# Optimization experiments

Measured on AMD Instinct MI355X. Metric: run time of the kernel, lower is better.

Reference implementation:

```python
import jax, jax.numpy as jnp
import numpy as np

N = 100000
E = 1000000
F_IN = 64
HID = 64
N_CLS = 2


def setup_inputs() -> dict:
    key = jax.random.key(0)
    ks = jax.random.split(key, 8)
    x = jax.random.normal(ks[0], (N, F_IN), dtype=jnp.float32)
    edge_index = jax.random.randint(ks[1], (2, E), 0, N, dtype=jnp.int64)
    s1 = 1.0 / np.sqrt(F_IN)
    s2 = 1.0 / np.sqrt(HID)
    # PyG SAGEConv: out = lin_l(mean_aggr) + lin_r(x); lin_l has bias, lin_r does not.
    W1l = jax.random.uniform(ks[2], (HID, F_IN), jnp.float32, -s1, s1)
    b1 = jax.random.uniform(ks[3], (HID,), jnp.float32, -s1, s1)
    W1r = jax.random.uniform(ks[4], (HID, F_IN), jnp.float32, -s1, s1)
    W2l = jax.random.uniform(ks[5], (N_CLS, HID), jnp.float32, -s2, s2)
    b2 = jax.random.uniform(ks[6], (N_CLS,), jnp.float32, -s2, s2)
    W2r = jax.random.uniform(ks[7], (N_CLS, HID), jnp.float32, -s2, s2)
    return {"x": x, "edge_index": edge_index, "W1l": W1l, "b1": b1,
            "W1r": W1r, "W2l": W2l, "b2": b2, "W2r": W2r}


def _mean_aggr(x, src, dst, n_nodes):
    # mean of source-node features over incoming edges per destination node
    summed = jax.ops.segment_sum(x[src], dst, num_segments=n_nodes)  # [N, F]
    cnt = jax.ops.segment_sum(jnp.ones((src.shape[0],), x.dtype), dst,
                              num_segments=n_nodes)
    return summed / jnp.maximum(cnt, 1.0)[:, None]


def _sage_conv(x, src, dst, Wl, Wr, b):
    aggr = _mean_aggr(x, src, dst, x.shape[0])
    out = aggr @ Wl.T + x @ Wr.T
    if b is not None:
        out = out + b
    return out


def reference(x, edge_index, W1l, b1, W1r, W2l, b2, W2r):
    src, dst = edge_index[0], edge_index[1]
    h = jax.nn.relu(_sage_conv(x, src, dst, W1l, W1r, b1))
    # F.dropout with training=False is identity (module evaluated in eval mode)
    out = _sage_conv(h, src, dst, W2l, W2r, b2)
    return (out, edge_index)
```

## Files before the change

kernel.cpp:

```cpp
#include <hip/hip_runtime.h>
#include <hip/hip_fp16.h>

#define NN 100000
#define NE 1000000
#define FD 64
#define CHK 64
#define NBUC 98
#define NHB 256
#define PB 3907
#define BCAP 12288

typedef _Float16 f16x2 __attribute__((ext_vector_type(2)));

#if defined(__has_builtin)
#if __has_builtin(__builtin_amdgcn_fdot2)
#define HAVE_FDOT2 1
#endif
#endif

__device__ __forceinline__ float fdot2f(__half2 a, __half2 b, float c) {
#ifdef HAVE_FDOT2
    return __builtin_amdgcn_fdot2(__builtin_bit_cast(f16x2, a),
                                  __builtin_bit_cast(f16x2, b), c, false);
#else
    const float2 af = __half22float2(a), bf = __half22float2(b);
    return c + af.x * bf.x + af.y * bf.y;
#endif
}

#define OFF_CNT  0
#define OFF_BSRC 128
#define OFF_BDST (OFF_BSRC + NBUC * BCAP)
#define OFF_ROW  (OFF_BDST + NBUC * BCAP / 2)
#define OFF_DEG  (OFF_ROW + NN)
#define OFF_CSR  (OFF_DEG + NN)
#define OFF_PQ   (OFF_CSR + NBUC * BCAP)
#define OFF_WTH  (OFF_PQ + 4 * NN)
#define OFF_XH   (OFF_WTH + 4096)

struct alignas(16) H8 { __half2 h[4]; };

#define NCC (NN * FD / 8)
#define NSTR (NCC + 8 + 2048)
#define NB4 (2 * NE / 4)
#define NTILE ((NN + CHK - 1) / CHK)
#define NEOB ((NB4 + 511) / 512)

__global__ __launch_bounds__(256) void k_bin(
    const int* __restrict__ ei, int* __restrict__ cnt,
    int* __restrict__ bsrc, unsigned short* __restrict__ bdstl,
    const float* __restrict__ x, __half* __restrict__ xh,
    const float* __restrict__ W1l, const float* __restrict__ W1r,
    __half2* __restrict__ wt1lh, __half2* __restrict__ wt1rh) {
    if (blockIdx.x < NHB) {
        __shared__ int h[NBUC];
        __shared__ int basep[NBUC];
        const int t = threadIdx.x;
        if (t < NBUC) h[t] = 0;
        __syncthreads();
        const int e0 = blockIdx.x * PB;
        const int e1 = min(e0 + PB, NE);
        for (int e = e0 + t; e < e1; e += 256)
            atomicAdd(&h[ei[NE + e] >> 10], 1);
        __syncthreads();
        if (t < NBUC) {
            const int c = h[t];
            basep[t] = c ? atomicAdd(&cnt[t], c) : 0;
            h[t] = 0;
        }
        __syncthreads();
        for (int e = e0 + t; e < e1; e += 256) {
            const int d = ei[NE + e];
            const int s = ei[e];
            const int k = d >> 10;
            const int r = atomicAdd(&h[k], 1);
            const int pos = k * BCAP + basep[k] + r;
            bsrc[pos] = s << 7;
            bdstl[pos] = (unsigned short)(d & 1023);
        }
        return;
    }
    const int tid = (blockIdx.x - NHB) * 256 + threadIdx.x;
    if (tid < NCC) {
        const float4 a = *((const float4*)x + (size_t)tid * 2);
        const float4 b = *((const float4*)x + (size_t)tid * 2 + 1);
        H8 o;
        o.h[0] = __floats2half2_rn(a.x, a.y);
        o.h[1] = __floats2half2_rn(a.z, a.w);
        o.h[2] = __floats2half2_rn(b.x, b.y);
        o.h[3] = __floats2half2_rn(b.z, b.w);
        *((H8*)xh + tid) = o;
    } else if (tid < NCC + 8) {
        H8 z;
        z.h[0] = z.h[1] = z.h[2] = z.h[3] = __float2half2_rn(0.f);
        *((H8*)(xh + (size_t)NN * FD) + (tid - NCC)) = z;
    } else if (tid < NSTR) {
        const int i = tid - (NCC + 8);
        const int j2 = i >> 6, k = i & 63;
        wt1lh[i] = __floats2half2_rn(W1l[k * FD + 2 * j2], W1l[k * FD + 2 * j2 + 1]);
        wt1rh[i] = __floats2half2_rn(W1r[k * FD + 2 * j2], W1r[k * FD + 2 * j2 + 1]);
    }
}

__global__ __launch_bounds__(1024) void k_D(const int* __restrict__ bsrc,
                                            const unsigned short* __restrict__ bdstl,
                                            const int* __restrict__ cnt,
                                            int* __restrict__ rowstart,
                                            int* __restrict__ deg,
                                            int* __restrict__ csr) {
    __shared__ int dcnt[1024];
    __shared__ int sc[1024];
    __shared__ int cur[1024];
    const int t = threadIdx.x;
    const int k = blockIdx.x;
    const int nbase = k << 10;
    const int eb0 = k * BCAP;
    const int fill = cnt[k];
    dcnt[t] = 0;
    __syncthreads();
    for (int e = t; e < fill; e += 1024)
        atomicAdd(&dcnt[bdstl[eb0 + e]], 1);
    __syncthreads();
    const int v = dcnt[t];
    sc[t] = v;
    __syncthreads();
    for (int off = 1; off < 1024; off <<= 1) {
        const int add = (t >= off) ? sc[t - off] : 0;
        __syncthreads();
        sc[t] += add;
        __syncthreads();
    }
    const int rsl = eb0 + sc[t] - v;
    cur[t] = rsl;
    if (nbase + t < NN) {
        rowstart[nbase + t] = rsl;
        deg[nbase + t] = v;
    }
    __syncthreads();
    for (int e = t; e < fill; e += 1024) {
        const int dl = bdstl[eb0 + e];
        const int pos = atomicAdd(&cur[dl], 1);
        csr[pos] = bsrc[eb0 + e];
    }
}

__global__ __launch_bounds__(512, 8) void k_l1(
    const int* __restrict__ csr, const int* __restrict__ rowstart,
    const int* __restrict__ deg, const __half* __restrict__ xh,
    const __half2* __restrict__ wt1lh, const float* __restrict__ b1,
    const __half2* __restrict__ wt1rh,
    const float* __restrict__ W2l, const float* __restrict__ b2,
    const float* __restrict__ W2r,
    float* __restrict__ pq,
    const int* __restrict__ ei, float* __restrict__ edge_out) {
    if (blockIdx.x >= NTILE) {
        const int i = (blockIdx.x - NTILE) * 512 + threadIdx.x;
        if (i < NB4) {
            const int4 v = *((const int4*)ei + i);
            float4 f;
            f.x = (float)v.x; f.y = (float)v.y; f.z = (float)v.z; f.w = (float)v.w;
            *((float4*)edge_out + i) = f;
        }
        return;
    }
    __shared__ __half2 sH[FD / 2][CHK + 1];
    __shared__ __half2 xH[FD / 2][CHK + 1];
    __shared__ float pacc[4 * CHK];
    const int lane = threadIdx.x & 63;
    const int wid = threadIdx.x >> 6;
    const int g = lane >> 3;
    const int sl = lane & 7;
    const int gb = g << 3;
    const int base = blockIdx.x * CHK;
    const char* xb = (const char*)xh;
    const unsigned slb = (unsigned)(sl << 4);
    const int ZOFF = NN << 7;

    if (threadIdx.x < 4 * CHK) pacc[threadIdx.x] = 0.f;

    const int nl = wid * 8 + g;
    const int n = base + nl;
    const bool ok = n < NN;
    const int nn = ok ? n : NN - 1;
    const int d = deg[nn];
    const int rs = rowstart[nn];

    int dmax = d;
    dmax = max(dmax, __shfl_xor(dmax, 8));
    dmax = max(dmax, __shfl_xor(dmax, 16));
    dmax = max(dmax, __shfl_xor(dmax, 32));
    const int nch = __builtin_amdgcn_readfirstlane((dmax + 7) >> 3);

    H8 acc;
    acc.h[0] = acc.h[1] = acc.h[2] = acc.h[3] = __float2half2_rn(0.f);

    for (int c = 0; c < nch; ++c) {
        const int jb = c << 3;
        const int ia = min(rs + jb + sl, NBUC * BCAP - 1);
        const int raw = csr[ia];
        const int offs = (jb + sl < d) ? raw : ZOFF;
        H8 buf[8];
#pragma unroll
        for (int t = 0; t < 8; ++t) {
            const unsigned ob = (unsigned)__shfl(offs, gb + t);
            buf[t] = *(const H8*)(xb + (size_t)(ob + slb));
        }
        __builtin_amdgcn_sched_barrier(0);
#pragma unroll
        for (int t = 0; t < 8; ++t) {
            acc.h[0] = __hadd2(acc.h[0], buf[t].h[0]);
            acc.h[1] = __hadd2(acc.h[1], buf[t].h[1]);
            acc.h[2] = __hadd2(acc.h[2], buf[t].h[2]);
            acc.h[3] = __hadd2(acc.h[3], buf[t].h[3]);
        }
    }

    if (ok) {
        const __half2 hinv = __float2half2_rn(1.0f / (float)max(d, 1));
        const H8 xv = *(const H8*)(xb + (size_t)(((unsigned)nn << 7) + slb));
#pragma unroll
        for (int t = 0; t < 4; ++t) {
            sH[sl * 4 + t][nl] = __hmul2(acc.h[t], hinv);
            xH[sl * 4 + t][nl] = xv.h[t];
        }
    }
    __syncthreads();

    const int kbase = __builtin_amdgcn_readfirstlane(wid * 8);
    float h[8];
#pragma unroll
    for (int t = 0; t < 8; ++t) h[t] = b1[kbase + t];
#pragma unroll 4
    for (int j2 = 0; j2 < FD / 2; ++j2) {
        const __half2 sj = sH[j2][lane];
        const __half2 xj = xH[j2][lane];
        const __half2* wl = wt1lh + j2 * FD + kbase;
        const __half2* wr = wt1rh + j2 * FD + kbase;
#pragma unroll
        for (int t = 0; t < 8; ++t) {
            h[t] = fdot2f(sj, wl[t], h[t]);
            h[t] = fdot2f(xj, wr[t], h[t]);
        }
    }

    float p0 = 0.f, p1 = 0.f, q0 = 0.f, q1 = 0.f;
#pragma unroll
    for (int t = 0; t < 8; ++t) {
        const float r = fmaxf(h[t], 0.f);
        p0 += r * W2l[kbase + t];
        p1 += r * W2l[FD + kbase + t];
        q0 += r * W2r[kbase + t];
        q1 += r * W2r[FD + kbase + t];
    }
    atomicAdd(&pacc[0 * CHK + lane], p0);
    atomicAdd(&pacc[1 * CHK + lane], p1);
    atomicAdd(&pacc[2 * CHK + lane], q0);
    atomicAdd(&pacc[3 * CHK + lane], q1);
    __syncthreads();

    {
        const int t = threadIdx.x;
        if (t < 4 * CHK) {
            const int nw = base + (t >> 2);
            if (nw < NN) {
                const int c = t & 3;
                float vv = pacc[c * CHK + (t >> 2)];
                if (c == 2) vv += b2[0];
                if (c == 3) vv += b2[1];
                pq[(size_t)nw * 4 + c] = vv;
            }
        }
    }
}

__global__ void k_l2(const int* __restrict__ csr, const int* __restrict__ rowstart,
                     const int* __restrict__ deg, const float* __restrict__ pq,
                     float* __restrict__ out) {
    const int gw = (blockIdx.x * blockDim.x + threadIdx.x) >> 6;
    const int lane = threadIdx.x & 63;
    const int sub = lane >> 4;
    const int sl = lane & 15;
    const int n = gw * 4 + sub;
    if (n >= NN) return;
    const int rs = rowstart[n];
    const int d = deg[n];
    const char* pb = (const char*)pq;
    float a0 = 0.f, a1 = 0.f;
    for (int i = sl; i < d; i += 16) {
        const unsigned v = (unsigned)csr[rs + i];
        const float2 p = *(const float2*)(pb + (size_t)(v >> 3));
        a0 += p.x;
        a1 += p.y;
    }
#pragma unroll
    for (int off = 8; off; off >>= 1) {
        a0 += __shfl_xor(a0, off);
        a1 += __shfl_xor(a1, off);
    }
    if (sl == 0) {
        const float inv = 1.0f / (float)max(d, 1);
        const float2 q = *(const float2*)(pq + 4 * (size_t)n + 2);
        *(float2*)(out + 2 * (size_t)n) = make_float2(a0 * inv + q.x, a1 * inv + q.y);
    }
}

extern "C" void kernel_launch(void* const* d_in, const int* in_sizes, int n_in,
                              void* d_out, int out_size, void* d_ws, size_t ws_size,
                              hipStream_t stream) {
    const float* x   = (const float*)d_in[0];
    const int*   ei  = (const int*)d_in[1];
    const float* W1l = (const float*)d_in[2];
    const float* b1  = (const float*)d_in[3];
    const float* W1r = (const float*)d_in[4];
    const float* W2l = (const float*)d_in[5];
    const float* b2  = (const float*)d_in[6];
    const float* W2r = (const float*)d_in[7];

    float* out      = (float*)d_out;
    float* edge_out = out + 2 * NN;

    int*    wsi      = (int*)d_ws;
    int*    cnt      = wsi + OFF_CNT;
    int*    bsrc     = wsi + OFF_BSRC;
    unsigned short* bdstl = (unsigned short*)(wsi + OFF_BDST);
    int*    rowstart = wsi + OFF_ROW;
    int*    deg      = wsi + OFF_DEG;
    int*    csr      = wsi + OFF_CSR;
    float*  pq       = (float*)d_ws + OFF_PQ;
    __half2* wt1lh   = (__half2*)((float*)d_ws + OFF_WTH);
    __half2* wt1rh   = wt1lh + 2048;
    __half*  xh      = (__half*)((float*)d_ws + OFF_XH);

    hipMemsetAsync(cnt, 0, 128 * sizeof(int), stream);

    const int nstrb = (NSTR + 255) / 256;
    k_bin<<<NHB + nstrb, 256, 0, stream>>>(ei, cnt, bsrc, bdstl, x, xh,
                                           W1l, W1r, wt1lh, wt1rh);
    k_D<<<NBUC, 1024, 0, stream>>>(bsrc, bdstl, cnt, rowstart, deg, csr);
    k_l1<<<NTILE + NEOB, 512, 0, stream>>>(csr, rowstart, deg, xh,
                                           wt1lh, b1, wt1rh,
                                           W2l, b2, W2r, pq, ei, edge_out);
    k_l2<<<((NN + 3) / 4 * 64 + 255) / 256, 256, 0, stream>>>(
        csr, rowstart, deg, pq, out);
}
```

Before: 108.6 us.

## Move fp16 conversion into CSR kernel and use wave-shuffle scan

The x/weight fp16 conversion blocks move from the binning kernel into the CSR-build kernel as extra 1024-thread blocks. They now run alongside the 98 lightly loaded CSR blocks instead of competing with the binning pass. The 1024-element Hillis-Steele shared-memory scan, which needed many block barriers, is replaced by a warp-shuffle scan plus a small cross-wave scan. The risk is that the conversion work now sits on the critical path of k_D, since k_bin becomes shorter.

```diff
diff --git a/kernel.cpp b/kernel.cpp
--- a/kernel.cpp
+++ b/kernel.cpp
@@ -42,76 +42,79 @@
 
 #define NCC (NN * FD / 8)
 #define NSTR (NCC + 8 + 2048)
+#define NSTRB ((NSTR + 1023) / 1024)
 #define NB4 (2 * NE / 4)
 #define NTILE ((NN + CHK - 1) / CHK)
 #define NEOB ((NB4 + 511) / 512)
 
 __global__ __launch_bounds__(256) void k_bin(
     const int* __restrict__ ei, int* __restrict__ cnt,
-    int* __restrict__ bsrc, unsigned short* __restrict__ bdstl,
+    int* __restrict__ bsrc, unsigned short* __restrict__ bdstl) {
+    __shared__ int h[NBUC];
+    __shared__ int basep[NBUC];
+    const int t = threadIdx.x;
+    if (t < NBUC) h[t] = 0;
+    __syncthreads();
+    const int e0 = blockIdx.x * PB;
+    const int e1 = min(e0 + PB, NE);
+    for (int e = e0 + t; e < e1; e += 256)
+        atomicAdd(&h[ei[NE + e] >> 10], 1);
+    __syncthreads();
+    if (t < NBUC) {
+        const int c = h[t];
+        basep[t] = c ? atomicAdd(&cnt[t], c) : 0;
+        h[t] = 0;
+    }
+    __syncthreads();
+    for (int e = e0 + t; e < e1; e += 256) {
+        const int d = ei[NE + e];
+        const int s = ei[e];
+        const int k = d >> 10;
+        const int r = atomicAdd(&h[k], 1);
+        const int pos = k * BCAP + basep[k] + r;
+        bsrc[pos] = s << 7;
+        bdstl[pos] = (unsigned short)(d & 1023);
+    }
+}
+
+__global__ __launch_bounds__(1024) void k_D(
+    const int* __restrict__ bsrc, const unsigned short* __restrict__ bdstl,
+    const int* __restrict__ cnt, int* __restrict__ rowstart,
+    int* __restrict__ deg, int* __restrict__ csr,
     const float* __restrict__ x, __half* __restrict__ xh,
     const float* __restrict__ W1l, const float* __restrict__ W1r,
     __half2* __restrict__ wt1lh, __half2* __restrict__ wt1rh) {
-    if (blockIdx.x < NHB) {
-        __shared__ int h[NBUC];
-        __shared__ int basep[NBUC];
-        const int t = threadIdx.x;
-        if (t < NBUC) h[t] = 0;
-        __syncthreads();
-        const int e0 = blockIdx.x * PB;
-        const int e1 = min(e0 + PB, NE);
-        for (int e = e0 + t; e < e1; e += 256)
-            atomicAdd(&h[ei[NE + e] >> 10], 1);
-        __syncthreads();
-        if (t < NBUC) {
-            const int c = h[t];
-            basep[t] = c ? atomicAdd(&cnt[t], c) : 0;
-            h[t] = 0;
-        }
-        __syncthreads();
-        for (int e = e0 + t; e < e1; e += 256) {
-            const int d = ei[NE + e];
-            const int s = ei[e];
-            const int k = d >> 10;
-            const int r = atomicAdd(&h[k], 1);
-            const int pos = k * BCAP + basep[k] + r;
-            bsrc[pos] = s << 7;
-            bdstl[pos] = (unsigned short)(d & 1023);
+    if (blockIdx.x >= NBUC) {
+        const int tid = (blockIdx.x - NBUC) * 1024 + threadIdx.x;
+        if (tid < NCC) {
+            const float4 a = *((const float4*)x + (size_t)tid * 2);
+            const float4 b = *((const float4*)x + (size_t)tid * 2 + 1);
+            H8 o;
+            o.h[0] = __floats2half2_rn(a.x, a.y);
+            o.h[1] = __floats2half2_rn(a.z, a.w);
+            o.h[2] = __floats2half2_rn(b.x, b.y);
+            o.h[3] = __floats2half2_rn(b.z, b.w);
+            *((H8*)xh + tid) = o;
+        } else if (tid < NCC + 8) {
+            H8 z;
+            z.h[0] = z.h[1] = z.h[2] = z.h[3] = __float2half2_rn(0.f);
+            *((H8*)(xh + (size_t)NN * FD) + (tid - NCC)) = z;
+        } else if (tid < NSTR) {
+            const int i = tid - (NCC + 8);
+            const int j2 = i >> 6, k = i & 63;
+            wt1lh[i] = __floats2half2_rn(W1l[k * FD + 2 * j2],
+                                         W1l[k * FD + 2 * j2 + 1]);
+            wt1rh[i] = __floats2half2_rn(W1r[k * FD + 2 * j2],
+                                         W1r[k * FD + 2 * j2 + 1]);
         }
         return;
     }
-    const int tid = (blockIdx.x - NHB) * 256 + threadIdx.x;
-    if (tid < NCC) {
-        const float4 a = *((const float4*)x + (size_t)tid * 2);
-        const float4 b = *((const float4*)x + (size_t)tid * 2 + 1);
-        H8 o;
-        o.h[0] = __floats2half2_rn(a.x, a.y);
-        o.h[1] = __floats2half2_rn(a.z, a.w);
-        o.h[2] = __floats2half2_rn(b.x, b.y);
-        o.h[3] = __floats2half2_rn(b.z, b.w);
-        *((H8*)xh + tid) = o;
-    } else if (tid < NCC + 8) {
-        H8 z;
-        z.h[0] = z.h[1] = z.h[2] = z.h[3] = __float2half2_rn(0.f);
-        *((H8*)(xh + (size_t)NN * FD) + (tid - NCC)) = z;
-    } else if (tid < NSTR) {
-        const int i = tid - (NCC + 8);
-        const int j2 = i >> 6, k = i & 63;
-        wt1lh[i] = __floats2half2_rn(W1l[k * FD + 2 * j2], W1l[k * FD + 2 * j2 + 1]);
-        wt1rh[i] = __floats2half2_rn(W1r[k * FD + 2 * j2], W1r[k * FD + 2 * j2 + 1]);
-    }
-}
-
-__global__ __launch_bounds__(1024) void k_D(const int* __restrict__ bsrc,
-                                            const unsigned short* __restrict__ bdstl,
-                                            const int* __restrict__ cnt,
-                                            int* __restrict__ rowstart,
-                                            int* __restrict__ deg,
-                                            int* __restrict__ csr) {
     __shared__ int dcnt[1024];
-    __shared__ int sc[1024];
     __shared__ int cur[1024];
+    __shared__ int wsum[16];
     const int t = threadIdx.x;
+    const int lane = t & 63;
+    const int wv = t >> 6;
     const int k = blockIdx.x;
     const int nbase = k << 10;
     const int eb0 = k * BCAP;
@@ -122,15 +125,26 @@
         atomicAdd(&dcnt[bdstl[eb0 + e]], 1);
     __syncthreads();
     const int v = dcnt[t];
-    sc[t] = v;
-    __syncthreads();
-    for (int off = 1; off < 1024; off <<= 1) {
-        const int add = (t >= off) ? sc[t - off] : 0;
-        __syncthreads();
-        sc[t] += add;
-        __syncthreads();
-    }
-    const int rsl = eb0 + sc[t] - v;
+    int inc = v;
+#pragma unroll
+    for (int off = 1; off < 64; off <<= 1) {
+        const int u = __shfl_up(inc, off);
+        if (lane >= off) inc += u;
+    }
+    if (lane == 63) wsum[wv] = inc;
+    __syncthreads();
+    if (t < 16) {
+        int s = wsum[t];
+#pragma unroll
+        for (int off = 1; off < 16; off <<= 1) {
+            const int u = __shfl_up(s, off);
+            if (t >= off) s += u;
+        }
+        wsum[t] = s;
+    }
+    __syncthreads();
+    const int woff = wv ? wsum[wv - 1] : 0;
+    const int rsl = eb0 + woff + inc - v;
     cur[t] = rsl;
     if (nbase + t < NN) {
         rowstart[nbase + t] = rsl;
@@ -333,10 +347,9 @@
 
     hipMemsetAsync(cnt, 0, 128 * sizeof(int), stream);
 
-    const int nstrb = (NSTR + 255) / 256;
-    k_bin<<<NHB + nstrb, 256, 0, stream>>>(ei, cnt, bsrc, bdstl, x, xh,
-                                           W1l, W1r, wt1lh, wt1rh);
-    k_D<<<NBUC, 1024, 0, stream>>>(bsrc, bdstl, cnt, rowstart, deg, csr);
+    k_bin<<<NHB, 256, 0, stream>>>(ei, cnt, bsrc, bdstl);
+    k_D<<<NBUC + NSTRB, 1024, 0, stream>>>(bsrc, bdstl, cnt, rowstart, deg, csr,
+                                           x, xh, W1l, W1r, wt1lh, wt1rh);
     k_l1<<<NTILE + NEOB, 512, 0, stream>>>(csr, rowstart, deg, xh,
                                            wt1lh, b1, wt1rh,
                                            W2l, b2, W2r, pq, ei, edge_out);
```

Result: no change. 107.7 us (-0.8%).
